# Optimization experiments

Measured on AMD Instinct MI355X. Metric: run time of the kernel, lower is better.

Reference implementation:

```python
import jax, jax.numpy as jnp
import numpy as np

N_HEADS, D_MODEL, D_HEAD = 16, 1024, 64
INIT_STD = 0.02
IGNORE = -100000.0


def setup_inputs() -> dict:
    key = jax.random.key(0)
    ks = jax.random.split(key, 5)
    x = jax.random.normal(ks[0], (2, 2048, D_MODEL), dtype=jnp.float32)
    W_Q = INIT_STD * jax.random.normal(ks[1], (N_HEADS, D_MODEL, D_HEAD), dtype=jnp.float32)
    W_K = INIT_STD * jax.random.normal(ks[2], (N_HEADS, D_MODEL, D_HEAD), dtype=jnp.float32)
    W_V = INIT_STD * jax.random.normal(ks[3], (N_HEADS, D_MODEL, D_HEAD), dtype=jnp.float32)
    W_O = INIT_STD * jax.random.normal(ks[4], (N_HEADS, D_HEAD, D_MODEL), dtype=jnp.float32)
    b_Q = jnp.zeros((N_HEADS, D_HEAD), dtype=jnp.float32)
    b_K = jnp.zeros((N_HEADS, D_HEAD), dtype=jnp.float32)
    b_V = jnp.zeros((N_HEADS, D_HEAD), dtype=jnp.float32)
    b_O = jnp.zeros((D_MODEL,), dtype=jnp.float32)
    return {"normalized_resid_pre": x, "W_Q": W_Q, "W_K": W_K, "W_V": W_V,
            "W_O": W_O, "b_Q": b_Q, "b_K": b_K, "b_V": b_V, "b_O": b_O}


def reference(normalized_resid_pre, W_Q, W_K, W_V, W_O, b_Q, b_K, b_V, b_O):
    x = normalized_resid_pre  # [b, s, d_model]
    q = jnp.einsum('bsm,hmd->bshd', x, W_Q) + b_Q  # [b, s, h, d_head]
    k = jnp.einsum('bsm,hmd->bshd', x, W_K) + b_K
    v = jnp.einsum('bsm,hmd->bshd', x, W_V) + b_V
    scores = jnp.einsum('bqhd,bkhd->bhqk', q, k) / jnp.sqrt(jnp.float32(D_HEAD))
    s = x.shape[1]
    causal = jnp.triu(jnp.ones((s, s), dtype=bool), k=1)  # True above diagonal
    scores = jnp.where(causal, jnp.float32(IGNORE), scores)
    pattern = jax.nn.softmax(scores, axis=-1)  # [b, h, q, k]
    z = jnp.einsum('bkhd,bhqk->bqhd', v, pattern)
    attn_out = jnp.einsum('bqhd,hdm->bqm', z, W_O) + b_O
    return attn_out
```

## Files before the change

### kernel.cpp

```cpp
#include <hip/hip_runtime.h>
#include <hip/hip_bf16.h>

#define BB   2
#define SS   2048
#define HH   16
#define DM_  1024
#define DH_  64
#define NROW 4096
#define NQKV 3072

typedef unsigned short u16;
typedef unsigned int u32;
using short4v = __attribute__((ext_vector_type(4))) short;
using short8 = __attribute__((ext_vector_type(8))) short;
using bf16x8 = __attribute__((ext_vector_type(8))) __bf16;
using f32x4  = __attribute__((ext_vector_type(4))) float;
using f32x16 = __attribute__((ext_vector_type(16))) float;

#define QSCALE 0.180336880f

__device__ __forceinline__ u16 f2bf(float f) {
    union { float f; unsigned u; } v; v.f = f;
    unsigned r = v.u + 0x7fffu + ((v.u >> 16) & 1u);
    return (u16)(r >> 16);
}

__device__ __forceinline__ f32x4 mfma16(bf16x8 a, bf16x8 b, f32x4 c) {
    return __builtin_amdgcn_mfma_f32_16x16x32_bf16(a, b, c, 0, 0, 0);
}
__device__ __forceinline__ f32x16 mfma32(bf16x8 a, bf16x8 b, f32x16 c) {
    return __builtin_amdgcn_mfma_f32_32x32x16_bf16(a, b, c, 0, 0, 0);
}

__device__ __forceinline__ u32 cvtpk(float lo, float hi) {
    u32 r;
    asm("v_cvt_pk_bf16_f32 %0, %1, %2" : "=v"(r) : "v"(lo), "v"(hi));
    return r;
}
#define PLSWAP(a, b) asm("v_permlane32_swap_b32 %0, %1" : "+v"(a), "+v"(b))

__device__ __forceinline__ void gload16(const void* g, void* l) {
    __builtin_amdgcn_global_load_lds(
        (const __attribute__((address_space(1))) void*)g,
        (__attribute__((address_space(3))) void*)l, 16, 0, 0);
}

__global__ __launch_bounds__(256)
void prep(const float* __restrict__ x,  const float* __restrict__ wq,
          const float* __restrict__ wk, const float* __restrict__ wv,
          const float* __restrict__ wo, const float* __restrict__ bq,
          const float* __restrict__ bk, const float* __restrict__ bv,
          u16* __restrict__ Xb, u16* __restrict__ Wt,
          u16* __restrict__ WoT, float* __restrict__ biasQKV) {
    __shared__ float tile[64][65];
    const int bx = blockIdx.x, t = threadIdx.x;
    if (bx < 512) {
        const int tid = bx * 256 + t;
        #pragma unroll
        for (int it = 0; it < 8; ++it) {
            int i = tid + it * 131072;
            float4 v = ((const float4*)x)[i];
            u16 b4[4] = {f2bf(v.x), f2bf(v.y), f2bf(v.z), f2bf(v.w)};
            ((short4v*)Xb)[i] = *(short4v*)b4;
        }
        if (tid < NQKV) {
            int mat = tid >> 10, h = (tid >> 6) & 15, d = tid & 63;
            const float* bb = (mat == 0) ? bq : ((mat == 1) ? bk : bv);
            biasQKV[tid] = bb[h * DH_ + d];
        }
    } else if (bx < 1280) {
        const int idx = bx - 512;
        const int m0 = (idx & 15) * 64, hm = idx >> 4;
        const int mat = hm >> 4, h = hm & 15;
        const float* w = (mat == 0) ? wq : ((mat == 1) ? wk : wv);
        #pragma unroll
        for (int it = 0; it < 4; ++it) {
            int row = it * 16 + (t >> 4), c4 = (t & 15) * 4;
            float4 v = *(const float4*)&w[((size_t)h * 1024 + m0 + row) * 64 + c4];
            tile[row][c4] = v.x; tile[row][c4 + 1] = v.y;
            tile[row][c4 + 2] = v.z; tile[row][c4 + 3] = v.w;
        }
        __syncthreads();
        #pragma unroll
        for (int it = 0; it < 2; ++it) {
            int c = it * 256 + t, d = c >> 3, mc = (c & 7) * 8;
            u16 buf[8];
            #pragma unroll
            for (int j = 0; j < 8; ++j) buf[j] = f2bf(tile[mc + j][d]);
            *(short8*)&Wt[((size_t)(mat * 1024 + h * 64 + d)) * 1024 + m0 + mc] = *(short8*)buf;
        }
    } else {
        const int idx = bx - 1280;
        const int n0 = (idx & 15) * 64, k0 = (idx >> 4) * 64;
        #pragma unroll
        for (int it = 0; it < 4; ++it) {
            int row = it * 16 + (t >> 4), c4 = (t & 15) * 4;
            float4 v = *(const float4*)&wo[(size_t)(k0 + row) * DM_ + n0 + c4];
            tile[row][c4] = v.x; tile[row][c4 + 1] = v.y;
            tile[row][c4 + 2] = v.z; tile[row][c4 + 3] = v.w;
        }
        __syncthreads();
        #pragma unroll
        for (int it = 0; it < 2; ++it) {
            int c = it * 256 + t, n = c >> 3, kc = (c & 7) * 8;
            u16 buf[8];
            #pragma unroll
            for (int j = 0; j < 8; ++j) buf[j] = f2bf(tile[kc + j][n]);
            *(short8*)&WoT[(size_t)(n0 + n) * DM_ + k0 + kc] = *(short8*)buf;
        }
    }
}

__device__ __forceinline__ void gemm_core_128(
    const u16* __restrict__ Ap, const u16* __restrict__ Bp,
    int brow, int bcol, u16* lds, f32x4 acc[4][2]) {
    const int t = threadIdx.x, l = t & 63;
    const int wid = t >> 6, wm = wid >> 2, wn = wid & 3;
    const int c0 = t, c1 = t + 512;
    const int r0 = c0 >> 3, sb0 = ((c0 & 7) ^ (r0 & 7)) << 3;
    const int r1 = c1 >> 3, sb1 = ((c1 & 7) ^ (r1 & 7)) << 3;
    u16* A0 = lds;
    u16* B0 = lds + 16384;
    const int rA0 = wm * 64 + (l & 15);
    const int rB0 = wn * 32 + (l & 15);
    const int sw  = (l & 7) << 3;
    const int colA = ((l >> 4) << 3);

    {
        gload16(Ap + (size_t)(brow + r0) * DM_ + sb0, A0 + c0 * 8);
        gload16(Ap + (size_t)(brow + r1) * DM_ + sb1, A0 + c1 * 8);
        gload16(Bp + (size_t)(bcol + r0) * DM_ + sb0, B0 + c0 * 8);
        gload16(Bp + (size_t)(bcol + r1) * DM_ + sb1, B0 + c1 * 8);
    }
    __syncthreads();
    for (int kt = 0; kt < 16; ++kt) {
        const int p = kt & 1;
        if (kt < 15) {
            const int ko = (kt + 1) * 64;
            gload16(Ap + (size_t)(brow + r0) * DM_ + ko + sb0, A0 + (p ^ 1) * 8192 + c0 * 8);
            gload16(Ap + (size_t)(brow + r1) * DM_ + ko + sb1, A0 + (p ^ 1) * 8192 + c1 * 8);
            gload16(Bp + (size_t)(bcol + r0) * DM_ + ko + sb0, B0 + (p ^ 1) * 8192 + c0 * 8);
            gload16(Bp + (size_t)(bcol + r1) * DM_ + ko + sb1, B0 + (p ^ 1) * 8192 + c1 * 8);
        }
        const u16* Ab = A0 + p * 8192;
        const u16* Bb = B0 + p * 8192;
        #pragma unroll
        for (int kc = 0; kc < 64; kc += 32) {
            const int cx = (kc + colA) ^ sw;
            bf16x8 af[4], bfr[2];
            #pragma unroll
            for (int m = 0; m < 4; ++m)
                af[m] = *(const bf16x8*)(Ab + (rA0 + m * 16) * 64 + cx);
            #pragma unroll
            for (int n = 0; n < 2; ++n)
                bfr[n] = *(const bf16x8*)(Bb + (rB0 + n * 16) * 64 + cx);
            __builtin_amdgcn_s_setprio(1);
            #pragma unroll
            for (int m = 0; m < 4; ++m)
                #pragma unroll
                for (int n = 0; n < 2; ++n)
                    acc[m][n] = mfma16(af[m], bfr[n], acc[m][n]);
            __builtin_amdgcn_s_setprio(0);
        }
        __syncthreads();
    }
}

__global__ __launch_bounds__(512)
void gemm_qkv3(const u16* __restrict__ Xb, const u16* __restrict__ Wt,
               const float* __restrict__ bias, u16* __restrict__ Qs,
               u16* __restrict__ Ks, u16* __restrict__ Vt) {
    __shared__ __align__(16) u16 lds[32768];
    const int bx = blockIdx.x, t = threadIdx.x, l = t & 63;
    const int wid = t >> 6, wm = wid >> 2, wn = wid & 3;
    f32x4 acc[4][2] = {};
    const bool isV = (bx >= 512);
    int brow, bcol; const u16 *Ap, *Bp;
    if (!isV) { brow = (bx & 31) * 128; bcol = (bx >> 5) * 128; Ap = Xb; Bp = Wt; }
    else { int i2 = bx - 512; brow = (i2 & 7) * 128; bcol = (i2 >> 3) * 128;
           Ap = Wt + (size_t)2048 * DM_; Bp = Xb; }
    gemm_core_128(Ap, Bp, brow, bcol, lds, acc);

    u16* wr_ = lds + wid * 2048;
    const int colbase = bcol + wn * 32;
    const int rowbase = brow + wm * 64;
    const int rsub = ((l >> 4) << 2);
    if (!isV) {
        const float b0 = bias[colbase + (l & 15)];
        const float b1 = bias[colbase + 16 + (l & 15)];
        const float scl = (colbase < 1024) ? QSCALE : 1.0f;
        #pragma unroll
        for (int m = 0; m < 4; ++m)
            #pragma unroll
            for (int n = 0; n < 2; ++n) {
                const float bb = n ? b1 : b0;
                #pragma unroll
                for (int r = 0; r < 4; ++r)
                    wr_[(m * 16 + rsub + r) * 32 + n * 16 + (l & 15)] =
                        f2bf((acc[m][n][r] + bb) * scl);
            }
    } else {
        #pragma unroll
        for (int m = 0; m < 4; ++m) {
            float4 bv = *(const float4*)&bias[2048 + rowbase + m * 16 + rsub];
            const float bbr[4] = {bv.x, bv.y, bv.z, bv.w};
            #pragma unroll
            for (int n = 0; n < 2; ++n)
                #pragma unroll
                for (int r = 0; r < 4; ++r)
                    wr_[(m * 16 + rsub + r) * 32 + n * 16 + (l & 15)] =
                        f2bf(acc[m][n][r] + bbr[r]);
        }
    }
    __syncthreads();
    if (!isV) {
        const int hsel = (colbase >> 6) & 15, d0 = colbase & 63;
        const int bsel = rowbase >> 11, s0 = rowbase & 2047;
        u16* outp = (colbase < 1024) ? Qs : Ks;
        #pragma unroll
        for (int p = 0; p < 4; ++p) {
            const int rr = p * 16 + (l >> 2);
            short8 v = *(const short8*)(wr_ + rr * 32 + (l & 3) * 8);
            *(short8*)&outp[(((size_t)bsel * HH + hsel) * SS + s0 + rr) * DH_ + d0 + (l & 3) * 8] = v;
        }
    } else {
        const int bsel = colbase >> 11, s0 = colbase & 2047;
        #pragma unroll
        for (int p = 0; p < 4; ++p) {
            const int rr = p * 16 + (l >> 2);
            short8 v = *(const short8*)(wr_ + rr * 32 + (l & 3) * 8);
            *(short8*)&Vt[((size_t)bsel * 1024 + rowbase + rr) * SS + s0 + (l & 3) * 8] = v;
        }
    }
}

__global__ __launch_bounds__(512)
void gemm_out3(const u16* __restrict__ Zb, const u16* __restrict__ WoT,
               const float* __restrict__ bO, float* __restrict__ out) {
    __shared__ __align__(16) u16 lds[32768];
    const int bx = blockIdx.x, t = threadIdx.x, l = t & 63;
    const int wid = t >> 6, wm = wid >> 2, wn = wid & 3;
    const int brow = (bx & 31) * 128, bcol = (bx >> 5) * 128;
    f32x4 acc[4][2] = {};
    gemm_core_128(Zb, WoT, brow, bcol, lds, acc);
    const int colbase = bcol + wn * 32;
    const int rowbase = brow + wm * 64;
    const int rsub = ((l >> 4) << 2);
    const float b0 = bO[colbase + (l & 15)];
    const float b1 = bO[colbase + 16 + (l & 15)];
    #pragma unroll
    for (int m = 0; m < 4; ++m)
        #pragma unroll
        for (int n = 0; n < 2; ++n) {
            const float bb = n ? b1 : b0;
            #pragma unroll
            for (int r = 0; r < 4; ++r)
                out[(size_t)(rowbase + m * 16 + rsub + r) * DM_ + colbase + n * 16 + (l & 15)] =
                    acc[m][n][r] + bb;
        }
}

__global__ __launch_bounds__(256)
void attn_fwd(const u16* __restrict__ Qs, const u16* __restrict__ Ks,
              const u16* __restrict__ Vt, u16* __restrict__ Zb) {
    __shared__ __align__(16) u16 fK[2][4096];
    __shared__ __align__(16) u16 fV[2][4096];
    __shared__ float lrL[128];
    const int bidx = blockIdx.x;
    const int qt = (bidx < 256) ? (15 - (bidx >> 5)) : ((bidx - 256) >> 5);
    const int bh = bidx & 31, b = bh >> 4, h = bh & 15;
    const int t = threadIdx.x, wid = t >> 6, l = t & 63;
    const int hi = l >> 5, c32 = l & 31;
    const u16* Qp = Qs + (size_t)bh * SS * DH_;
    const u16* Kp = Ks + (size_t)bh * SS * DH_;
    const u16* Vp = Vt + (size_t)bh * DH_ * SS;
    const int qw = qt * 128 + wid * 32;
    const int nt = 2 * qt + 2;

    bf16x8 aq[4];
    #pragma unroll
    for (int dk = 0; dk < 4; ++dk)
        aq[dk] = *(const bf16x8*)&Qp[(size_t)(qw + c32) * DH_ + dk * 16 + hi * 8];

    int kOff[2]; size_t vOff[2]; int dst[2];
    #pragma unroll
    for (int i = 0; i < 2; ++i) {
        const int c = t + 256 * i, sec = c >> 6, ln = c & 63;
        kOff[i] = ((sec >> 2) * 32 + (ln & 31)) * DH_ + (sec & 3) * 16 + (ln >> 5) * 8;
        vOff[i] = (size_t)((sec >> 2) * 32 + (ln & 31)) * SS + (sec & 3) * 16 + (ln >> 5) * 8;
        dst[i] = c * 8;
    }

    short8 kA[2], vA[2];
    #pragma unroll
    for (int i = 0; i < 2; ++i) {
        kA[i] = *(const short8*)(Kp + kOff[i]);
        vA[i] = *(const short8*)(Vp + vOff[i]);
    }
    #pragma unroll
    for (int i = 0; i < 2; ++i) {
        *(short8*)(&fK[0][dst[i]]) = kA[i];
        *(short8*)(&fV[0][dst[i]]) = vA[i];
    }
    if (nt > 1) {
        #pragma unroll
        for (int i = 0; i < 2; ++i) {
            kA[i] = *(const short8*)(Kp + (size_t)64 * DH_ + kOff[i]);
            vA[i] = *(const short8*)(Vp + 64 + vOff[i]);
        }
    }
    __syncthreads();

    f32x16 o0 = {}, o1 = {};
    float lrow = 0.f;

    for (int kt = 0; kt < nt; ++kt) {
        const int p = kt & 1;
        if (kt + 1 < nt) {
            #pragma unroll
            for (int i = 0; i < 2; ++i) {
                *(short8*)(&fK[p ^ 1][dst[i]]) = kA[i];
                *(short8*)(&fV[p ^ 1][dst[i]]) = vA[i];
            }
            if (kt + 2 < nt) {
                const int nb = (kt + 2) * 64;
                #pragma unroll
                for (int i = 0; i < 2; ++i) {
                    kA[i] = *(const short8*)(Kp + (size_t)nb * DH_ + kOff[i]);
                    vA[i] = *(const short8*)(Vp + nb + vOff[i]);
                }
            }
        }
        const int kv0 = kt * 64;
        if (kv0 <= qw + 31) {
            const u16* fKb = fK[p];
            const u16* fVb = fV[p];
            const bool have1 = (kv0 + 32 <= qw + 31);
            f32x16 s0 = {}, s1 = {};
            __builtin_amdgcn_s_setprio(1);
            #pragma unroll
            for (int dk = 0; dk < 4; ++dk)
                s0 = mfma32(*(const bf16x8*)(fKb + dk * 512 + l * 8), aq[dk], s0);
            if (have1) {
                #pragma unroll
                for (int dk = 0; dk < 4; ++dk)
                    s1 = mfma32(*(const bf16x8*)(fKb + (4 + dk) * 512 + l * 8), aq[dk], s1);
            }
            __builtin_amdgcn_s_setprio(0);
            if (kv0 + 63 > qw) {
                const int q = qw + c32;
                #pragma unroll
                for (int r = 0; r < 16; ++r) {
                    const int crow = (r & 3) + 8 * (r >> 2) + 4 * hi;
                    if (kv0 + crow > q) s0[r] = -1e30f;
                }
                if (have1) {
                    #pragma unroll
                    for (int r = 0; r < 16; ++r) {
                        const int crow = (r & 3) + 8 * (r >> 2) + 4 * hi;
                        if (kv0 + 32 + crow > q) s1[r] = -1e30f;
                    }
                }
            }
            #pragma unroll
            for (int r = 0; r < 16; ++r) { s0[r] = exp2f(s0[r]); lrow += s0[r]; }
            if (have1) {
                #pragma unroll
                for (int r = 0; r < 16; ++r) { s1[r] = exp2f(s1[r]); lrow += s1[r]; }
            }
            __builtin_amdgcn_s_setprio(1);
            #define PV_STEP(PS, B8, KS)                                          \
            {                                                                    \
                u32 cA  = cvtpk(PS[B8 + 0], PS[B8 + 1]);                         \
                u32 cA2 = cvtpk(PS[B8 + 2], PS[B8 + 3]);                         \
                u32 cB  = cvtpk(PS[B8 + 4], PS[B8 + 5]);                         \
                u32 cB2 = cvtpk(PS[B8 + 6], PS[B8 + 7]);                         \
                PLSWAP(cA, cB); PLSWAP(cA2, cB2);                                \
                u32 w[4] = {cA, cA2, cB, cB2};                                   \
                bf16x8 pa = *(bf16x8*)w;                                         \
                o0 = mfma32(pa, *(const bf16x8*)(fVb + (0 * 4 + (KS)) * 512 + l * 8), o0); \
                o1 = mfma32(pa, *(const bf16x8*)(fVb + (1 * 4 + (KS)) * 512 + l * 8), o1); \
            }
            PV_STEP(s0, 0, 0)
            PV_STEP(s0, 8, 1)
            if (have1) {
                PV_STEP(s1, 0, 2)
                PV_STEP(s1, 8, 3)
            }
            #undef PV_STEP
            __builtin_amdgcn_s_setprio(0);
        }
        __syncthreads();
    }

    lrow += __shfl_xor(lrow, 32);
    lrL[wid * 32 + c32] = lrow;
    float invv[16];
    #pragma unroll
    for (int g = 0; g < 4; ++g) {
        float4 lv = *(const float4*)&lrL[wid * 32 + 8 * g + 4 * hi];
        invv[g * 4 + 0] = 1.0f / lv.x;
        invv[g * 4 + 1] = 1.0f / lv.y;
        invv[g * 4 + 2] = 1.0f / lv.z;
        invv[g * 4 + 3] = 1.0f / lv.w;
    }
    #pragma unroll
    for (int r = 0; r < 16; ++r) {
        const int q = qw + (r & 3) + 8 * (r >> 2) + 4 * hi;
        u16* zp = &Zb[(((size_t)b * SS + q) * HH + h) * DH_];
        zp[c32]      = f2bf(o0[r] * invv[r]);
        zp[32 + c32] = f2bf(o1[r] * invv[r]);
    }
}

extern "C" void kernel_launch(void* const* d_in, const int* in_sizes, int n_in,
                              void* d_out, int out_size, void* d_ws, size_t ws_size,
                              hipStream_t stream) {
    const float* x  = (const float*)d_in[0];
    const float* wq = (const float*)d_in[1];
    const float* wk = (const float*)d_in[2];
    const float* wv = (const float*)d_in[3];
    const float* wo = (const float*)d_in[4];
    const float* bq = (const float*)d_in[5];
    const float* bk = (const float*)d_in[6];
    const float* bv = (const float*)d_in[7];
    const float* bO = (const float*)d_in[8];
    float* out = (float*)d_out;

    char* w = (char*)d_ws;
    u16* Xb  = (u16*)w;  w += (size_t)NROW * DM_ * 2;
    u16* Wt  = (u16*)w;  w += (size_t)NQKV * DM_ * 2;
    u16* WoT = (u16*)w;  w += (size_t)DM_ * DM_ * 2;
    float* biasQKV = (float*)w; w += (size_t)NQKV * 4;
    u16* Qs  = (u16*)w;  w += (size_t)BB * HH * SS * DH_ * 2;
    u16* Ks  = (u16*)w;  w += (size_t)BB * HH * SS * DH_ * 2;
    u16* Vt  = (u16*)w;  w += (size_t)BB * HH * SS * DH_ * 2;
    u16* Zb  = (u16*)w;  w += (size_t)BB * HH * SS * DH_ * 2;

    prep<<<1536, 256, 0, stream>>>(x, wq, wk, wv, wo, bq, bk, bv,
                                   Xb, Wt, WoT, biasQKV);
    gemm_qkv3<<<768, 512, 0, stream>>>(Xb, Wt, biasQKV, Qs, Ks, Vt);
    attn_fwd<<<512, 256, 0, stream>>>(Qs, Ks, Vt, Zb);
    gemm_out3<<<256, 512, 0, stream>>>(Zb, WoT, bO, out);
}
```

Baseline: 102.6 us.

## Split attention KV range across wave pairs with LDS merge and direct-to-LDS loads

Result: faster. 97.00 us (-5.5%).

```diff
diff --git a/kernel.cpp b/kernel.cpp
--- a/kernel.cpp
+++ b/kernel.cpp
@@ -38,6 +38,14 @@
     return r;
 }
 #define PLSWAP(a, b) asm("v_permlane32_swap_b32 %0, %1" : "+v"(a), "+v"(b))
+
+__device__ __forceinline__ float fexp2(float x) {
+#if __has_builtin(__builtin_amdgcn_exp2f)
+    return __builtin_amdgcn_exp2f(x);
+#else
+    float r; asm("v_exp_f32 %0, %1" : "=v"(r) : "v"(x)); return r;
+#endif
+}
 
 __device__ __forceinline__ void gload16(const void* g, void* l) {
     __builtin_amdgcn_global_load_lds(
@@ -260,81 +268,58 @@
         }
 }
 
-__global__ __launch_bounds__(256)
+__global__ __launch_bounds__(256, 4)
 void attn_fwd(const u16* __restrict__ Qs, const u16* __restrict__ Ks,
               const u16* __restrict__ Vt, u16* __restrict__ Zb) {
-    __shared__ __align__(16) u16 fK[2][4096];
-    __shared__ __align__(16) u16 fV[2][4096];
-    __shared__ float lrL[128];
+    __shared__ __align__(16) u16 fKV[16384];
+    __shared__ __align__(16) float lrP[64];
+    __shared__ __align__(16) float lrX[64];
     const int bidx = blockIdx.x;
-    const int qt = (bidx < 256) ? (15 - (bidx >> 5)) : ((bidx - 256) >> 5);
+    const int j  = (bidx < 512) ? (31 - (bidx >> 5)) : ((bidx - 512) >> 5);
     const int bh = bidx & 31, b = bh >> 4, h = bh & 15;
     const int t = threadIdx.x, wid = t >> 6, l = t & 63;
     const int hi = l >> 5, c32 = l & 31;
+    const int qh = wid >> 1, par = wid & 1, wp = qh;
     const u16* Qp = Qs + (size_t)bh * SS * DH_;
     const u16* Kp = Ks + (size_t)bh * SS * DH_;
     const u16* Vp = Vt + (size_t)bh * DH_ * SS;
-    const int qw = qt * 128 + wid * 32;
-    const int nt = 2 * qt + 2;
+    const int qw = j * 64 + qh * 32;
+    const int nr = (j >> 1) + 1;
 
     bf16x8 aq[4];
     #pragma unroll
     for (int dk = 0; dk < 4; ++dk)
         aq[dk] = *(const bf16x8*)&Qp[(size_t)(qw + c32) * DH_ + dk * 16 + hi * 8];
 
-    int kOff[2]; size_t vOff[2]; int dst[2];
+    int kOff[2]; size_t vOff[2]; int dstc[2];
     #pragma unroll
     for (int i = 0; i < 2; ++i) {
         const int c = t + 256 * i, sec = c >> 6, ln = c & 63;
         kOff[i] = ((sec >> 2) * 32 + (ln & 31)) * DH_ + (sec & 3) * 16 + (ln >> 5) * 8;
         vOff[i] = (size_t)((sec >> 2) * 32 + (ln & 31)) * SS + (sec & 3) * 16 + (ln >> 5) * 8;
-        dst[i] = c * 8;
-    }
-
-    short8 kA[2], vA[2];
-    #pragma unroll
-    for (int i = 0; i < 2; ++i) {
-        kA[i] = *(const short8*)(Kp + kOff[i]);
-        vA[i] = *(const short8*)(Vp + vOff[i]);
-    }
-    #pragma unroll
-    for (int i = 0; i < 2; ++i) {
-        *(short8*)(&fK[0][dst[i]]) = kA[i];
-        *(short8*)(&fV[0][dst[i]]) = vA[i];
-    }
-    if (nt > 1) {
+        dstc[i] = c * 8;
+    }
+    u16* fK0 = fKV;          u16* fK1 = fKV + 4096;
+    u16* fV0 = fKV + 8192;   u16* fV1 = fKV + 12288;
+    const u16* fKb = par ? fK1 : fK0;
+    const u16* fVb = par ? fV1 : fV0;
+
+    f32x16 o0 = {}, o1 = {};
+    float lrp[4] = {0.f, 0.f, 0.f, 0.f};
+
+    for (int r = 0; r < nr; ++r) {
+        const int k0a = r * 128, k0b = r * 128 + 64;
+        __syncthreads();
         #pragma unroll
         for (int i = 0; i < 2; ++i) {
-            kA[i] = *(const short8*)(Kp + (size_t)64 * DH_ + kOff[i]);
-            vA[i] = *(const short8*)(Vp + 64 + vOff[i]);
-        }
-    }
-    __syncthreads();
-
-    f32x16 o0 = {}, o1 = {};
-    float lrow = 0.f;
-
-    for (int kt = 0; kt < nt; ++kt) {
-        const int p = kt & 1;
-        if (kt + 1 < nt) {
-            #pragma unroll
-            for (int i = 0; i < 2; ++i) {
-                *(short8*)(&fK[p ^ 1][dst[i]]) = kA[i];
-                *(short8*)(&fV[p ^ 1][dst[i]]) = vA[i];
-            }
-            if (kt + 2 < nt) {
-                const int nb = (kt + 2) * 64;
-                #pragma unroll
-                for (int i = 0; i < 2; ++i) {
-                    kA[i] = *(const short8*)(Kp + (size_t)nb * DH_ + kOff[i]);
-                    vA[i] = *(const short8*)(Vp + nb + vOff[i]);
-                }
-            }
-        }
-        const int kv0 = kt * 64;
+            gload16(Kp + (size_t)k0a * DH_ + kOff[i], fK0 + dstc[i]);
+            gload16(Kp + (size_t)k0b * DH_ + kOff[i], fK1 + dstc[i]);
+            gload16(Vp + k0a + vOff[i], fV0 + dstc[i]);
+            gload16(Vp + k0b + vOff[i], fV1 + dstc[i]);
+        }
+        __syncthreads();
+        const int kv0 = r * 128 + par * 64;
         if (kv0 <= qw + 31) {
-            const u16* fKb = fK[p];
-            const u16* fVb = fV[p];
             const bool have1 = (kv0 + 32 <= qw + 31);
             f32x16 s0 = {}, s1 = {};
             __builtin_amdgcn_s_setprio(1);
@@ -350,23 +335,29 @@
             if (kv0 + 63 > qw) {
                 const int q = qw + c32;
                 #pragma unroll
-                for (int r = 0; r < 16; ++r) {
-                    const int crow = (r & 3) + 8 * (r >> 2) + 4 * hi;
-                    if (kv0 + crow > q) s0[r] = -1e30f;
+                for (int r16 = 0; r16 < 16; ++r16) {
+                    const int crow = (r16 & 3) + 8 * (r16 >> 2) + 4 * hi;
+                    if (kv0 + crow > q) s0[r16] = -1e30f;
                 }
                 if (have1) {
                     #pragma unroll
-                    for (int r = 0; r < 16; ++r) {
-                        const int crow = (r & 3) + 8 * (r >> 2) + 4 * hi;
-                        if (kv0 + 32 + crow > q) s1[r] = -1e30f;
+                    for (int r16 = 0; r16 < 16; ++r16) {
+                        const int crow = (r16 & 3) + 8 * (r16 >> 2) + 4 * hi;
+                        if (kv0 + 32 + crow > q) s1[r16] = -1e30f;
                     }
                 }
             }
             #pragma unroll
-            for (int r = 0; r < 16; ++r) { s0[r] = exp2f(s0[r]); lrow += s0[r]; }
+            for (int r16 = 0; r16 < 16; ++r16) {
+                s0[r16] = fexp2(s0[r16]);
+                lrp[r16 & 3] += s0[r16];
+            }
             if (have1) {
                 #pragma unroll
-                for (int r = 0; r < 16; ++r) { s1[r] = exp2f(s1[r]); lrow += s1[r]; }
+                for (int r16 = 0; r16 < 16; ++r16) {
+                    s1[r16] = fexp2(s1[r16]);
+                    lrp[r16 & 3] += s1[r16];
+                }
             }
             __builtin_amdgcn_s_setprio(1);
             #define PV_STEP(PS, B8, KS)                                          \
@@ -390,26 +381,43 @@
             #undef PV_STEP
             __builtin_amdgcn_s_setprio(0);
         }
-        __syncthreads();
-    }
-
+    }
+    float lrow = (lrp[0] + lrp[1]) + (lrp[2] + lrp[3]);
     lrow += __shfl_xor(lrow, 32);
-    lrL[wid * 32 + c32] = lrow;
-    float invv[16];
-    #pragma unroll
-    for (int g = 0; g < 4; ++g) {
-        float4 lv = *(const float4*)&lrL[wid * 32 + 8 * g + 4 * hi];
-        invv[g * 4 + 0] = 1.0f / lv.x;
-        invv[g * 4 + 1] = 1.0f / lv.y;
-        invv[g * 4 + 2] = 1.0f / lv.z;
-        invv[g * 4 + 3] = 1.0f / lv.w;
-    }
-    #pragma unroll
-    for (int r = 0; r < 16; ++r) {
-        const int q = qw + (r & 3) + 8 * (r >> 2) + 4 * hi;
-        u16* zp = &Zb[(((size_t)b * SS + q) * HH + h) * DH_];
-        zp[c32]      = f2bf(o0[r] * invv[r]);
-        zp[32 + c32] = f2bf(o1[r] * invv[r]);
+
+    float* mrg = (float*)fKV;
+    __syncthreads();
+    if (par) {
+        #pragma unroll
+        for (int e = 0; e < 16; ++e) mrg[wp * 2048 + e * 64 + l] = o0[e];
+        #pragma unroll
+        for (int e = 0; e < 16; ++e) mrg[wp * 2048 + (16 + e) * 64 + l] = o1[e];
+        if (hi == 0) lrP[wp * 32 + c32] = lrow;
+    }
+    __syncthreads();
+    if (!par) {
+        #pragma unroll
+        for (int e = 0; e < 16; ++e) o0[e] += mrg[wp * 2048 + e * 64 + l];
+        #pragma unroll
+        for (int e = 0; e < 16; ++e) o1[e] += mrg[wp * 2048 + (16 + e) * 64 + l];
+        lrow += lrP[wp * 32 + c32];
+        lrX[wp * 32 + c32] = lrow;
+        float invv[16];
+        #pragma unroll
+        for (int g = 0; g < 4; ++g) {
+            float4 lv = *(const float4*)&lrX[wp * 32 + 8 * g + 4 * hi];
+            invv[g * 4 + 0] = 1.0f / lv.x;
+            invv[g * 4 + 1] = 1.0f / lv.y;
+            invv[g * 4 + 2] = 1.0f / lv.z;
+            invv[g * 4 + 3] = 1.0f / lv.w;
+        }
+        #pragma unroll
+        for (int r16 = 0; r16 < 16; ++r16) {
+            const int q = qw + (r16 & 3) + 8 * (r16 >> 2) + 4 * hi;
+            u16* zp = &Zb[(((size_t)b * SS + q) * HH + h) * DH_];
+            zp[c32]      = f2bf(o0[r16] * invv[r16]);
+            zp[32 + c32] = f2bf(o1[r16] * invv[r16]);
+        }
     }
 }
 
@@ -440,6 +448,6 @@
     prep<<<1536, 256, 0, stream>>>(x, wq, wk, wv, wo, bq, bk, bv,
                                    Xb, Wt, WoT, biasQKV);
     gemm_qkv3<<<768, 512, 0, stream>>>(Xb, Wt, biasQKV, Qs, Ks, Vt);
-    attn_fwd<<<512, 256, 0, stream>>>(Qs, Ks, Vt, Zb);
+    attn_fwd<<<1024, 256, 0, stream>>>(Qs, Ks, Vt, Zb);
     gemm_out3<<<256, 512, 0, stream>>>(Zb, WoT, bO, out);
 }
```
